# Performance work log

Measured on AMD Instinct MI355X. Metric: run time of the kernel, lower is better.

The kernel has to match this reference:

```python
import jax, jax.numpy as jnp
import numpy as np

# unit constants from Converter._set_unit (astropy values, precomputed):
# unit_nu_f_nu = Lsun / (4*pi*(10 pc)^2) in erg/s/cm^2
UNIT_NU_F_NU = 3.1995e-07
# unit_f_nu = unit_nu_f_nu / (c / angstrom) in Jy
UNIT_F_NU = 1.0673e-02


def setup_inputs() -> dict:
    key = jax.random.key(0)
    k1, k2 = jax.random.split(key)
    B, F, L = 8192, 128, 8192
    # strictly increasing wavelength grid in Angstrom
    lam = 100.0 + 6.0 * (jnp.arange(L, dtype=jnp.float32) + 1.0)
    # positive fluxes so log10 is defined
    l_target = jax.random.uniform(k1, (B, L), dtype=jnp.float32) + 0.1
    # filter transmissions (already unit-normalized in __init__); keep positive
    trans_filter = 1e-3 * (jax.random.uniform(k2, (F, L), dtype=jnp.float32) + 0.01)
    return {"l_target": l_target, "trans_filter": trans_filter, "lam": lam, "return_ph": 1}


def reference(l_target, trans_filter, lam, return_ph):
    if return_ph:
        # trapz(y, x) == sum_l y[l] * w[l] with trapezoid weights w from lam.
        dx = jnp.diff(lam)  # [L-1]
        w = jnp.zeros_like(lam).at[:-1].add(0.5 * dx).at[1:].add(0.5 * dx)  # [L]
        # fuse weights into the filter matrix -> single GEMM, no [B,F,L] intermediate
        wt = trans_filter * w[None, :]  # [F, L]
        flux = jnp.einsum('bl,fl->bf', l_target, wt)  # [B, F]
        return -2.5 * jnp.log10(flux)
    else:
        return l_target * lam[None, :] * UNIT_F_NU
```

## Files before the change

kernel.cpp:

```cpp
#include <hip/hip_runtime.h>
#include <hip/hip_bf16.h>
#include <cstdint>

#define B_ROWS 8192
#define F_FILT 128
#define L_LEN  8192
#define SPLITK 8
#define KCHUNK (L_LEN / SPLITK)
#define NSTEPS (KCHUNK / 32)
#define WM     32
#define WAVES  4
#define BM     (WM * WAVES)

typedef __attribute__((ext_vector_type(4))) float f32x4;
typedef __attribute__((ext_vector_type(8))) short bf16x8;

__device__ __forceinline__ short f2bf(float f) {
  union { float f; unsigned u; } v; v.f = f;
  unsigned u = v.u + 0x7FFFu + ((v.u >> 16) & 1u);
  return (short)(u >> 16);
}

__device__ __forceinline__ bf16x8 cvt8(f32x4 x, f32x4 y) {
  bf16x8 r;
  r[0] = f2bf(x[0]); r[1] = f2bf(x[1]); r[2] = f2bf(x[2]); r[3] = f2bf(x[3]);
  r[4] = f2bf(y[0]); r[5] = f2bf(y[1]); r[6] = f2bf(y[2]); r[7] = f2bf(y[3]);
  return r;
}

__global__ void build_wt(const float* __restrict__ trans,
                         const float* __restrict__ lam,
                         ushort* __restrict__ wt) {
  int idx = blockIdx.x * blockDim.x + threadIdx.x;
  int l = idx & (L_LEN - 1);
  float lo = (l > 0)         ? lam[l - 1] : lam[0];
  float hi = (l < L_LEN - 1) ? lam[l + 1] : lam[L_LEN - 1];
  float w = 0.5f * (hi - lo);
  wt[idx] = (ushort)f2bf(trans[idx] * w);
}

__global__ __launch_bounds__(256, 2)
void gemm_splitk(const float* __restrict__ A,
                 const ushort* __restrict__ WT,
                 float* __restrict__ P ) {
  const int lane = threadIdx.x & 63;
  const int wave = threadIdx.x >> 6;
  const int rl = lane & 15;
  const int kg = lane >> 4;
  const int m0 = blockIdx.x * BM + wave * WM;
  const int s  = blockIdx.y;
  const int k0 = s * KCHUNK;

  const float*  pa = A  + (size_t)(m0 + rl) * L_LEN + k0 + kg * 8;
  const ushort* pb = WT + (size_t)rl        * L_LEN + k0 + kg * 8;

  f32x4 acc[2][8] = {};

  f32x4 a_cur[2][2];
  bf16x8 b_cur[8];

  auto loadA = [&](int kk, f32x4 a[2][2]) {
#pragma unroll
    for (int t = 0; t < 2; ++t) {
      const float* p = pa + (size_t)t * 16 * L_LEN + kk;
      a[t][0] = __builtin_nontemporal_load((const f32x4*)p);
      a[t][1] = __builtin_nontemporal_load((const f32x4*)(p + 4));
    }
  };
  auto loadB = [&](int kk, bf16x8 b[8]) {
#pragma unroll
    for (int j = 0; j < 8; ++j)
      b[j] = *(const bf16x8*)(pb + (size_t)j * 16 * L_LEN + kk);
  };
  auto compute = [&](f32x4 a[2][2], bf16x8 b[8]) {
    bf16x8 af0 = cvt8(a[0][0], a[0][1]);
    bf16x8 af1 = cvt8(a[1][0], a[1][1]);
#pragma unroll
    for (int j = 0; j < 8; ++j) {
      acc[0][j] = __builtin_amdgcn_mfma_f32_16x16x32_bf16(af0, b[j], acc[0][j], 0, 0, 0);
      acc[1][j] = __builtin_amdgcn_mfma_f32_16x16x32_bf16(af1, b[j], acc[1][j], 0, 0, 0);
    }
  };

  loadA(0, a_cur);
  loadB(0, b_cur);
#pragma unroll 1
  for (int step = 0; step < NSTEPS - 1; ++step) {
    f32x4 a_nxt[2][2]; bf16x8 b_nxt[8];
    loadA((step + 1) * 32, a_nxt);
    loadB((step + 1) * 32, b_nxt);
    compute(a_cur, b_cur);
#pragma unroll
    for (int t = 0; t < 2; ++t) { a_cur[t][0] = a_nxt[t][0]; a_cur[t][1] = a_nxt[t][1]; }
#pragma unroll
    for (int j = 0; j < 8; ++j) b_cur[j] = b_nxt[j];
  }
  compute(a_cur, b_cur);

  float* po = P + ((size_t)s * B_ROWS + m0) * F_FILT;
#pragma unroll
  for (int t = 0; t < 2; ++t) {
#pragma unroll
    for (int r = 0; r < 4; ++r) {
      int row = t * 16 + kg * 4 + r;
#pragma unroll
      for (int j = 0; j < 8; ++j)
        po[(size_t)row * F_FILT + j * 16 + rl] = acc[t][j][r];
    }
  }
}

__global__ void finish(const float* __restrict__ P, float* __restrict__ out) {
  int idx = blockIdx.x * blockDim.x + threadIdx.x;
  float s = 0.f;
#pragma unroll
  for (int i = 0; i < SPLITK; ++i)
    s += P[(size_t)i * ((size_t)B_ROWS * F_FILT) + idx];
  out[idx] = -2.5f * log10f(s);
}

extern "C" void kernel_launch(void* const* d_in, const int* in_sizes, int n_in,
                              void* d_out, int out_size, void* d_ws, size_t ws_size,
                              hipStream_t stream) {
  const float* A    = (const float*)d_in[0];
  const float* T    = (const float*)d_in[1];
  const float* lam  = (const float*)d_in[2];

  ushort* wt = (ushort*)d_ws;
  float*  P  = (float*)((char*)d_ws + (size_t)F_FILT * L_LEN * sizeof(ushort));
  float*  out = (float*)d_out;

  build_wt<<<(F_FILT * L_LEN) / 256, 256, 0, stream>>>(T, lam, wt);
  gemm_splitk<<<dim3(B_ROWS / BM, SPLITK), 256, 0, stream>>>(A, wt, P);
  finish<<<(B_ROWS * F_FILT) / 256, 256, 0, stream>>>(P, out);
}
```

Baseline: 426.4 us.

## Stage A and filter tiles through double-buffered LDS in split-K GEMM

The GEMM now loads 64-wide K chunks of A and of the weighted filter matrix cooperatively into double-buffered shared memory, converting A to bf16 on store. Before, each wave fetched the full filter tile from global memory, so the B traffic was repeated four times per block. The change also replaces per-lane strided loads with wider contiguous loads. It adds LDS usage and a barrier per chunk, and with about 55KB of LDS per block the two-blocks-per-CU occupancy target may no longer be reachable.

After: 428.8 us. About the same (+0.6%).

```diff
diff --git a/kernel.cpp b/kernel.cpp
--- a/kernel.cpp
+++ b/kernel.cpp
@@ -7,10 +7,12 @@
 #define L_LEN  8192
 #define SPLITK 8
 #define KCHUNK (L_LEN / SPLITK)
-#define NSTEPS (KCHUNK / 32)
+#define BK     64
+#define CHUNKS (KCHUNK / BK)
 #define WM     32
 #define WAVES  4
 #define BM     (WM * WAVES)
+#define LDP    72
 
 typedef __attribute__((ext_vector_type(4))) float f32x4;
 typedef __attribute__((ext_vector_type(8))) short bf16x8;
@@ -43,66 +45,94 @@
 void gemm_splitk(const float* __restrict__ A,
                  const ushort* __restrict__ WT,
                  float* __restrict__ P ) {
-  const int lane = threadIdx.x & 63;
-  const int wave = threadIdx.x >> 6;
+  __shared__ ushort sA[2][BM][LDP];
+  __shared__ ushort sB[2][F_FILT][LDP];
+
+  const int tid  = threadIdx.x;
+  const int lane = tid & 63;
+  const int wave = tid >> 6;
   const int rl = lane & 15;
   const int kg = lane >> 4;
-  const int m0 = blockIdx.x * BM + wave * WM;
+  const int m0 = blockIdx.x * BM;
   const int s  = blockIdx.y;
   const int k0 = s * KCHUNK;
 
-  const float*  pa = A  + (size_t)(m0 + rl) * L_LEN + k0 + kg * 8;
-  const ushort* pb = WT + (size_t)rl        * L_LEN + k0 + kg * 8;
+  const int ar = lane >> 2;
+  const int aq = lane & 3;
+  const int br = tid >> 3;
+  const int bc = tid & 7;
 
   f32x4 acc[2][8] = {};
 
-  f32x4 a_cur[2][2];
-  bf16x8 b_cur[8];
+  f32x4  axr[2][4];
+  bf16x8 bxr[4];
 
-  auto loadA = [&](int kk, f32x4 a[2][2]) {
+  auto stage_load = [&](int c) {
+    const int kc = k0 + c * BK;
 #pragma unroll
-    for (int t = 0; t < 2; ++t) {
-      const float* p = pa + (size_t)t * 16 * L_LEN + kk;
-      a[t][0] = __builtin_nontemporal_load((const f32x4*)p);
-      a[t][1] = __builtin_nontemporal_load((const f32x4*)(p + 4));
+    for (int r2 = 0; r2 < 2; ++r2) {
+      const int row = wave * WM + r2 * 16 + ar;
+      const float* p = A + (size_t)(m0 + row) * L_LEN + kc + aq * 16;
+      axr[r2][0] = *(const f32x4*)(p);
+      axr[r2][1] = *(const f32x4*)(p + 4);
+      axr[r2][2] = *(const f32x4*)(p + 8);
+      axr[r2][3] = *(const f32x4*)(p + 12);
     }
-  };
-  auto loadB = [&](int kk, bf16x8 b[8]) {
 #pragma unroll
-    for (int j = 0; j < 8; ++j)
-      b[j] = *(const bf16x8*)(pb + (size_t)j * 16 * L_LEN + kk);
-  };
-  auto compute = [&](f32x4 a[2][2], bf16x8 b[8]) {
-    bf16x8 af0 = cvt8(a[0][0], a[0][1]);
-    bf16x8 af1 = cvt8(a[1][0], a[1][1]);
-#pragma unroll
-    for (int j = 0; j < 8; ++j) {
-      acc[0][j] = __builtin_amdgcn_mfma_f32_16x16x32_bf16(af0, b[j], acc[0][j], 0, 0, 0);
-      acc[1][j] = __builtin_amdgcn_mfma_f32_16x16x32_bf16(af1, b[j], acc[1][j], 0, 0, 0);
+    for (int r4 = 0; r4 < 4; ++r4) {
+      const int row = r4 * 32 + br;
+      bxr[r4] = *(const bf16x8*)(WT + (size_t)row * L_LEN + kc + bc * 8);
     }
   };
 
-  loadA(0, a_cur);
-  loadB(0, b_cur);
+  auto stage_store = [&](int buf) {
+#pragma unroll
+    for (int r2 = 0; r2 < 2; ++r2) {
+      const int row = wave * WM + r2 * 16 + ar;
+      ushort* d = &sA[buf][row][aq * 16];
+      *(bf16x8*)(d)     = cvt8(axr[r2][0], axr[r2][1]);
+      *(bf16x8*)(d + 8) = cvt8(axr[r2][2], axr[r2][3]);
+    }
+#pragma unroll
+    for (int r4 = 0; r4 < 4; ++r4) {
+      const int row = r4 * 32 + br;
+      *(bf16x8*)(&sB[buf][row][bc * 8]) = bxr[r4];
+    }
+  };
+
+  auto compute = [&](int buf) {
+#pragma unroll
+    for (int st = 0; st < 2; ++st) {
+      const int off = st * 32 + kg * 8;
+      bf16x8 a0 = *(const bf16x8*)(&sA[buf][wave * WM + rl][off]);
+      bf16x8 a1 = *(const bf16x8*)(&sA[buf][wave * WM + 16 + rl][off]);
+#pragma unroll
+      for (int j = 0; j < 8; ++j) {
+        bf16x8 b = *(const bf16x8*)(&sB[buf][j * 16 + rl][off]);
+        acc[0][j] = __builtin_amdgcn_mfma_f32_16x16x32_bf16(a0, b, acc[0][j], 0, 0, 0);
+        acc[1][j] = __builtin_amdgcn_mfma_f32_16x16x32_bf16(a1, b, acc[1][j], 0, 0, 0);
+      }
+    }
+  };
+
+  stage_load(0);
+  stage_store(0);
+  __syncthreads();
 #pragma unroll 1
-  for (int step = 0; step < NSTEPS - 1; ++step) {
-    f32x4 a_nxt[2][2]; bf16x8 b_nxt[8];
-    loadA((step + 1) * 32, a_nxt);
-    loadB((step + 1) * 32, b_nxt);
-    compute(a_cur, b_cur);
-#pragma unroll
-    for (int t = 0; t < 2; ++t) { a_cur[t][0] = a_nxt[t][0]; a_cur[t][1] = a_nxt[t][1]; }
-#pragma unroll
-    for (int j = 0; j < 8; ++j) b_cur[j] = b_nxt[j];
+  for (int c = 0; c < CHUNKS; ++c) {
+    const bool pre = (c + 1 < CHUNKS);
+    if (pre) stage_load(c + 1);
+    compute(c & 1);
+    if (pre) stage_store((c + 1) & 1);
+    __syncthreads();
   }
-  compute(a_cur, b_cur);
 
-  float* po = P + ((size_t)s * B_ROWS + m0) * F_FILT;
+  float* po = P + ((size_t)s * B_ROWS + m0 + wave * WM) * F_FILT;
 #pragma unroll
   for (int t = 0; t < 2; ++t) {
 #pragma unroll
     for (int r = 0; r < 4; ++r) {
-      int row = t * 16 + kg * 4 + r;
+      const int row = t * 16 + kg * 4 + r;
 #pragma unroll
       for (int j = 0; j < 8; ++j)
         po[(size_t)row * F_FILT + j * 16 + rl] = acc[t][j][r];
```

## Stage A through LDS as bf16 with coalesced row loads and register prefetch

Applied to the files above, without the earlier changes.

The GEMM kernel now loads fp32 A rows with each lane covering four contiguous floats, so row reads are fully coalesced. It converts them to bf16 and stores them in a double-buffered, padded LDS tile, then reads MFMA fragments back from LDS, while prefetching the next A chunk into registers two chunks ahead. Split-K drops from 8 to 4 and blocks shrink to two waves, which also cuts partial-sum traffic. The cost is a very large register prefetch buffer, a large LDS footprint and far fewer resident waves per CU, which may limit latency hiding. The filter matrix is still read from global memory on every step with no reuse.

After: 476.5 us. 11.8% more time.

```diff
diff --git a/kernel.cpp b/kernel.cpp
--- a/kernel.cpp
+++ b/kernel.cpp
@@ -5,27 +5,23 @@
 #define B_ROWS 8192
 #define F_FILT 128
 #define L_LEN  8192
-#define SPLITK 8
+#define SPLITK 4
 #define KCHUNK (L_LEN / SPLITK)
-#define NSTEPS (KCHUNK / 32)
+#define BK     256
+#define CHUNKS (KCHUNK / BK)
+#define WAVES  2
 #define WM     32
-#define WAVES  4
 #define BM     (WM * WAVES)
+#define LDP    264
 
 typedef __attribute__((ext_vector_type(4))) float f32x4;
 typedef __attribute__((ext_vector_type(8))) short bf16x8;
+typedef __attribute__((ext_vector_type(4))) short bf16x4;
 
 __device__ __forceinline__ short f2bf(float f) {
   union { float f; unsigned u; } v; v.f = f;
   unsigned u = v.u + 0x7FFFu + ((v.u >> 16) & 1u);
   return (short)(u >> 16);
-}
-
-__device__ __forceinline__ bf16x8 cvt8(f32x4 x, f32x4 y) {
-  bf16x8 r;
-  r[0] = f2bf(x[0]); r[1] = f2bf(x[1]); r[2] = f2bf(x[2]); r[3] = f2bf(x[3]);
-  r[4] = f2bf(y[0]); r[5] = f2bf(y[1]); r[6] = f2bf(y[2]); r[7] = f2bf(y[3]);
-  return r;
 }
 
 __global__ void build_wt(const float* __restrict__ trans,
@@ -39,70 +35,75 @@
   wt[idx] = (ushort)f2bf(trans[idx] * w);
 }
 
-__global__ __launch_bounds__(256, 2)
+__global__ __launch_bounds__(128, 1)
 void gemm_splitk(const float* __restrict__ A,
                  const ushort* __restrict__ WT,
                  float* __restrict__ P ) {
+  __shared__ ushort sA[2][BM][LDP];
+
   const int lane = threadIdx.x & 63;
   const int wave = threadIdx.x >> 6;
   const int rl = lane & 15;
   const int kg = lane >> 4;
-  const int m0 = blockIdx.x * BM + wave * WM;
+  const int m0 = blockIdx.x * BM;
   const int s  = blockIdx.y;
   const int k0 = s * KCHUNK;
-
-  const float*  pa = A  + (size_t)(m0 + rl) * L_LEN + k0 + kg * 8;
-  const ushort* pb = WT + (size_t)rl        * L_LEN + k0 + kg * 8;
+  const int rowbase = wave * WM;
 
   f32x4 acc[2][8] = {};
+  f32x4 bnk[2][WM];
 
-  f32x4 a_cur[2][2];
-  bf16x8 b_cur[8];
+  const float* pa = A + (size_t)(m0 + rowbase) * L_LEN + k0 + (lane << 2);
 
-  auto loadA = [&](int kk, f32x4 a[2][2]) {
+  auto issueA = [&](int c, int b) {
+    const float* p = pa + c * BK;
 #pragma unroll
-    for (int t = 0; t < 2; ++t) {
-      const float* p = pa + (size_t)t * 16 * L_LEN + kk;
-      a[t][0] = __builtin_nontemporal_load((const f32x4*)p);
-      a[t][1] = __builtin_nontemporal_load((const f32x4*)(p + 4));
-    }
+    for (int r = 0; r < WM; ++r)
+      bnk[b][r] = *(const f32x4*)(p + (size_t)r * L_LEN);
   };
-  auto loadB = [&](int kk, bf16x8 b[8]) {
+
+  auto storeA = [&](int b, int buf) {
 #pragma unroll
-    for (int j = 0; j < 8; ++j)
-      b[j] = *(const bf16x8*)(pb + (size_t)j * 16 * L_LEN + kk);
-  };
-  auto compute = [&](f32x4 a[2][2], bf16x8 b[8]) {
-    bf16x8 af0 = cvt8(a[0][0], a[0][1]);
-    bf16x8 af1 = cvt8(a[1][0], a[1][1]);
-#pragma unroll
-    for (int j = 0; j < 8; ++j) {
-      acc[0][j] = __builtin_amdgcn_mfma_f32_16x16x32_bf16(af0, b[j], acc[0][j], 0, 0, 0);
-      acc[1][j] = __builtin_amdgcn_mfma_f32_16x16x32_bf16(af1, b[j], acc[1][j], 0, 0, 0);
+    for (int r = 0; r < WM; ++r) {
+      f32x4 v = bnk[b][r];
+      bf16x4 h;
+      h[0] = f2bf(v[0]); h[1] = f2bf(v[1]); h[2] = f2bf(v[2]); h[3] = f2bf(v[3]);
+      *(bf16x4*)(&sA[buf][rowbase + r][lane << 2]) = h;
     }
   };
 
-  loadA(0, a_cur);
-  loadB(0, b_cur);
+  auto compute = [&](int buf, int c) {
+    const ushort* pb = WT + k0 + c * BK;
+#pragma unroll
+    for (int st = 0; st < BK / 32; ++st) {
+      const int off = st * 32 + kg * 8;
+      bf16x8 a0 = *(const bf16x8*)(&sA[buf][rowbase + rl][off]);
+      bf16x8 a1 = *(const bf16x8*)(&sA[buf][rowbase + 16 + rl][off]);
+#pragma unroll
+      for (int j = 0; j < 8; ++j) {
+        bf16x8 b = *(const bf16x8*)(pb + (size_t)(j * 16 + rl) * L_LEN + off);
+        acc[0][j] = __builtin_amdgcn_mfma_f32_16x16x32_bf16(a0, b, acc[0][j], 0, 0, 0);
+        acc[1][j] = __builtin_amdgcn_mfma_f32_16x16x32_bf16(a1, b, acc[1][j], 0, 0, 0);
+      }
+    }
+  };
+
+  issueA(0, 0);
+  issueA(1, 1);
+  storeA(0, 0);
 #pragma unroll 1
-  for (int step = 0; step < NSTEPS - 1; ++step) {
-    f32x4 a_nxt[2][2]; bf16x8 b_nxt[8];
-    loadA((step + 1) * 32, a_nxt);
-    loadB((step + 1) * 32, b_nxt);
-    compute(a_cur, b_cur);
-#pragma unroll
-    for (int t = 0; t < 2; ++t) { a_cur[t][0] = a_nxt[t][0]; a_cur[t][1] = a_nxt[t][1]; }
-#pragma unroll
-    for (int j = 0; j < 8; ++j) b_cur[j] = b_nxt[j];
+  for (int c = 0; c < CHUNKS; ++c) {
+    compute(c & 1, c);
+    if (c + 2 < CHUNKS) issueA(c + 2, c & 1);
+    if (c + 1 < CHUNKS) storeA((c + 1) & 1, (c + 1) & 1);
   }
-  compute(a_cur, b_cur);
 
-  float* po = P + ((size_t)s * B_ROWS + m0) * F_FILT;
+  float* po = P + ((size_t)s * B_ROWS + m0 + rowbase) * F_FILT;
 #pragma unroll
   for (int t = 0; t < 2; ++t) {
 #pragma unroll
     for (int r = 0; r < 4; ++r) {
-      int row = t * 16 + kg * 4 + r;
+      const int row = t * 16 + kg * 4 + r;
 #pragma unroll
       for (int j = 0; j < 8; ++j)
         po[(size_t)row * F_FILT + j * 16 + rl] = acc[t][j][r];
@@ -131,6 +132,6 @@
   float*  out = (float*)d_out;
 
   build_wt<<<(F_FILT * L_LEN) / 256, 256, 0, stream>>>(T, lam, wt);
-  gemm_splitk<<<dim3(B_ROWS / BM, SPLITK), 256, 0, stream>>>(A, wt, P);
+  gemm_splitk<<<dim3(B_ROWS / BM, SPLITK), 128, 0, stream>>>(A, wt, P);
   finish<<<(B_ROWS * F_FILT) / 256, 256, 0, stream>>>(P, out);
 }
```

## Pre-pack filter weights into MFMA fragment layout and shrink GEMM tiles

Applied to the files above, without the earlier changes.

The weighted filter matrix is now built directly in a packed per-lane bf16x8 fragment order, so each wave reads B operands as one contiguous 16-byte load per lane instead of strided rows. The GEMM tile shrinks to 16 rows per wave and 2 waves per block, split-K doubles to 16, and the inner loop is fully unrolled with a simpler A-only register prefetch. This aims to raise occupancy and coalescing. In exchange it doubles the partial-sum buffer that the finish kernel must reduce, and each B fragment is reused by half as many rows.

After: 425.5 us. Within noise of the previous version (-0.2%).

```diff
diff --git a/kernel.cpp b/kernel.cpp
--- a/kernel.cpp
+++ b/kernel.cpp
@@ -5,12 +5,13 @@
 #define B_ROWS 8192
 #define F_FILT 128
 #define L_LEN  8192
-#define SPLITK 8
+#define SPLITK 16
 #define KCHUNK (L_LEN / SPLITK)
-#define NSTEPS (KCHUNK / 32)
-#define WM     32
-#define WAVES  4
+#define STEPS  (KCHUNK / 32)
+#define WM     16
+#define WAVES  2
 #define BM     (WM * WAVES)
+#define MBLK   (B_ROWS / BM)
 
 typedef __attribute__((ext_vector_type(4))) float f32x4;
 typedef __attribute__((ext_vector_type(8))) short bf16x8;
@@ -30,18 +31,25 @@
 
 __global__ void build_wt(const float* __restrict__ trans,
                          const float* __restrict__ lam,
-                         ushort* __restrict__ wt) {
-  int idx = blockIdx.x * blockDim.x + threadIdx.x;
-  int l = idx & (L_LEN - 1);
-  float lo = (l > 0)         ? lam[l - 1] : lam[0];
-  float hi = (l < L_LEN - 1) ? lam[l + 1] : lam[L_LEN - 1];
-  float w = 0.5f * (hi - lo);
-  wt[idx] = (ushort)f2bf(trans[idx] * w);
+                         ushort* __restrict__ bp) {
+  int o = blockIdx.x * blockDim.x + threadIdx.x;
+  int lane = o & 63, j = (o >> 6) & 7, gs = o >> 9;
+  int f = j * 16 + (lane & 15);
+  int k = gs * 32 + (lane >> 4) * 8;
+  bf16x8 h;
+#pragma unroll
+  for (int i = 0; i < 8; ++i) {
+    int l = k + i;
+    float lo = (l > 0)         ? lam[l - 1] : lam[0];
+    float hi = (l < L_LEN - 1) ? lam[l + 1] : lam[L_LEN - 1];
+    h[i] = f2bf(trans[(size_t)f * L_LEN + l] * (0.5f * (hi - lo)));
+  }
+  *(bf16x8*)(bp + (size_t)o * 8) = h;
 }
 
-__global__ __launch_bounds__(256, 2)
+__global__ __launch_bounds__(128, 4)
 void gemm_splitk(const float* __restrict__ A,
-                 const ushort* __restrict__ WT,
+                 const ushort* __restrict__ BP,
                  float* __restrict__ P ) {
   const int lane = threadIdx.x & 63;
   const int wave = threadIdx.x >> 6;
@@ -52,61 +60,37 @@
   const int k0 = s * KCHUNK;
 
   const float*  pa = A  + (size_t)(m0 + rl) * L_LEN + k0 + kg * 8;
-  const ushort* pb = WT + (size_t)rl        * L_LEN + k0 + kg * 8;
+  const ushort* pb = BP + ((size_t)(k0 / 32) * 512 + lane) * 8;
 
-  f32x4 acc[2][8] = {};
+  f32x4 acc[8] = {};
 
-  f32x4 a_cur[2][2];
-  bf16x8 b_cur[8];
+  f32x4 an0 = *(const f32x4*)pa;
+  f32x4 an1 = *(const f32x4*)(pa + 4);
 
-  auto loadA = [&](int kk, f32x4 a[2][2]) {
 #pragma unroll
-    for (int t = 0; t < 2; ++t) {
-      const float* p = pa + (size_t)t * 16 * L_LEN + kk;
-      a[t][0] = __builtin_nontemporal_load((const f32x4*)p);
-      a[t][1] = __builtin_nontemporal_load((const f32x4*)(p + 4));
+  for (int st = 0; st < STEPS; ++st) {
+    f32x4 ac0 = an0, ac1 = an1;
+    if (st + 1 < STEPS) {
+      const float* p = pa + (st + 1) * 32;
+      an0 = *(const f32x4*)p;
+      an1 = *(const f32x4*)(p + 4);
     }
-  };
-  auto loadB = [&](int kk, bf16x8 b[8]) {
-#pragma unroll
-    for (int j = 0; j < 8; ++j)
-      b[j] = *(const bf16x8*)(pb + (size_t)j * 16 * L_LEN + kk);
-  };
-  auto compute = [&](f32x4 a[2][2], bf16x8 b[8]) {
-    bf16x8 af0 = cvt8(a[0][0], a[0][1]);
-    bf16x8 af1 = cvt8(a[1][0], a[1][1]);
+    bf16x8 af = cvt8(ac0, ac1);
+    const ushort* pbs = pb + (size_t)st * 4096;
 #pragma unroll
     for (int j = 0; j < 8; ++j) {
-      acc[0][j] = __builtin_amdgcn_mfma_f32_16x16x32_bf16(af0, b[j], acc[0][j], 0, 0, 0);
-      acc[1][j] = __builtin_amdgcn_mfma_f32_16x16x32_bf16(af1, b[j], acc[1][j], 0, 0, 0);
+      bf16x8 b = *(const bf16x8*)(pbs + (size_t)j * 512);
+      acc[j] = __builtin_amdgcn_mfma_f32_16x16x32_bf16(af, b, acc[j], 0, 0, 0);
     }
-  };
-
-  loadA(0, a_cur);
-  loadB(0, b_cur);
-#pragma unroll 1
-  for (int step = 0; step < NSTEPS - 1; ++step) {
-    f32x4 a_nxt[2][2]; bf16x8 b_nxt[8];
-    loadA((step + 1) * 32, a_nxt);
-    loadB((step + 1) * 32, b_nxt);
-    compute(a_cur, b_cur);
-#pragma unroll
-    for (int t = 0; t < 2; ++t) { a_cur[t][0] = a_nxt[t][0]; a_cur[t][1] = a_nxt[t][1]; }
-#pragma unroll
-    for (int j = 0; j < 8; ++j) b_cur[j] = b_nxt[j];
   }
-  compute(a_cur, b_cur);
 
   float* po = P + ((size_t)s * B_ROWS + m0) * F_FILT;
 #pragma unroll
-  for (int t = 0; t < 2; ++t) {
+  for (int r = 0; r < 4; ++r) {
+    const int row = kg * 4 + r;
 #pragma unroll
-    for (int r = 0; r < 4; ++r) {
-      int row = t * 16 + kg * 4 + r;
-#pragma unroll
-      for (int j = 0; j < 8; ++j)
-        po[(size_t)row * F_FILT + j * 16 + rl] = acc[t][j][r];
-    }
+    for (int j = 0; j < 8; ++j)
+      po[(size_t)row * F_FILT + j * 16 + rl] = acc[j][r];
   }
 }
 
@@ -126,11 +110,11 @@
   const float* T    = (const float*)d_in[1];
   const float* lam  = (const float*)d_in[2];
 
-  ushort* wt = (ushort*)d_ws;
+  ushort* bp = (ushort*)d_ws;
   float*  P  = (float*)((char*)d_ws + (size_t)F_FILT * L_LEN * sizeof(ushort));
   float*  out = (float*)d_out;
 
-  build_wt<<<(F_FILT * L_LEN) / 256, 256, 0, stream>>>(T, lam, wt);
-  gemm_splitk<<<dim3(B_ROWS / BM, SPLITK), 256, 0, stream>>>(A, wt, P);
+  build_wt<<<(F_FILT * L_LEN / 8) / 256, 256, 0, stream>>>(T, lam, bp);
+  gemm_splitk<<<dim3(MBLK, SPLITK), 128, 0, stream>>>(A, bp, P);
   finish<<<(B_ROWS * F_FILT) / 256, 256, 0, stream>>>(P, out);
 }
```
